# Kernel tuning notes

Hardware: AMD Instinct MI355X
Metric: run time of the kernel (lower is better)

Reference implementation:

```python
import jax, jax.numpy as jnp
import numpy as np

D_MODEL = 2048
H_TOTAL = 32
D_HEAD = D_MODEL // H_TOTAL  # 64
H_ACTIVE = 4
ROPE_BASE = 10000.0


def _apply_rope(t, cos, sin):
    # t: [B, H, T, DH]; cos/sin: [T, DH//2]; interleaved pair rotation
    t1 = t[..., 0::2]
    t2 = t[..., 1::2]
    r1 = t1 * cos - t2 * sin
    r2 = t1 * sin + t2 * cos
    return jnp.stack([r1, r2], axis=-1).reshape(t.shape)


def setup_inputs() -> dict:
    key = jax.random.key(0)
    ks = jax.random.split(key, 4)
    x = jax.random.normal(ks[0], (4, 1024, D_MODEL), dtype=jnp.float32)
    w_router = jax.random.normal(ks[1], (D_MODEL, H_TOTAL), dtype=jnp.float32) * 0.02
    w_qkv = jax.random.normal(ks[2], (D_MODEL, 3 * D_MODEL), dtype=jnp.float32) * 0.02
    w_out = jax.random.normal(ks[3], (D_MODEL, D_MODEL), dtype=jnp.float32) * 0.02
    return {"x": x, "w_router": w_router, "w_qkv": w_qkv, "w_out": w_out}


def reference(x, w_router, w_qkv, w_out):
    B, T, _ = x.shape
    # --- SwitchRouter: per-token probabilities over heads ---
    probs = jax.nn.softmax(x @ w_router, axis=-1)            # [B, T, H]
    # top-h_active heads per token (dense-math equivalent of sparse dispatch)
    _, top_idx = jax.lax.top_k(probs, H_ACTIVE)              # [B, T, HA]
    mask = jnp.sum(jax.nn.one_hot(top_idx, H_TOTAL, dtype=x.dtype), axis=-2)  # [B, T, H]
    gate = probs * mask                                      # router-scored gate

    # --- QKV projection ---
    qkv = x @ w_qkv                                          # [B, T, 3D]
    q, k, v = jnp.split(qkv, 3, axis=-1)
    def to_heads(t):
        return t.reshape(B, T, H_TOTAL, D_HEAD).transpose(0, 2, 1, 3)  # [B, H, T, DH]
    q, k, v = to_heads(q), to_heads(k), to_heads(v)

    # --- RoPE ---
    inv_freq = 1.0 / (ROPE_BASE ** (jnp.arange(0, D_HEAD, 2, dtype=jnp.float32) / D_HEAD))
    ang = jnp.arange(T, dtype=jnp.float32)[:, None] * inv_freq[None, :]  # [T, DH/2]
    cos, sin = jnp.cos(ang), jnp.sin(ang)
    q = _apply_rope(q, cos, sin)
    k = _apply_rope(k, cos, sin)

    # --- causal SDPA ---
    scores = jnp.einsum('bhqd,bhkd->bhqk', q, k) / np.float32(np.sqrt(D_HEAD))
    causal = jnp.tril(jnp.ones((T, T), dtype=bool))
    scores = jnp.where(causal, scores, jnp.finfo(scores.dtype).min)
    attn = jax.nn.softmax(scores, axis=-1)
    out = jnp.einsum('bhqk,bhkd->bhqd', attn, v)             # [B, H, T, DH]

    # --- gate: only active heads contribute (scatter-back equivalent) ---
    out = out * gate.transpose(0, 2, 1)[..., None]           # [B, H, T, DH]
    out = out.transpose(0, 2, 1, 3).reshape(B, T, D_MODEL)
    return out @ w_out
```

## Files before the change

### kernel.cpp

```cpp
#include <hip/hip_runtime.h>
#include <hip/hip_bf16.h>
#include <stdint.h>
#include <stddef.h>

typedef __attribute__((ext_vector_type(8))) short bf16x8;
typedef __attribute__((ext_vector_type(8))) unsigned short u16x8;
typedef __attribute__((ext_vector_type(4))) float f32x4;

#define TT 1024

__device__ __forceinline__ unsigned short f2bf(float f){
  unsigned u = __builtin_bit_cast(unsigned, f);
  unsigned r = 0x7fffu + ((u >> 16) & 1u);
  return (unsigned short)((u + r) >> 16);
}
__device__ __forceinline__ float bf2f(unsigned short s){
  unsigned u = ((unsigned)s) << 16;
  return __builtin_bit_cast(float, u);
}
__device__ __forceinline__ void gload16(const unsigned short* g, unsigned short* l){
  __builtin_amdgcn_global_load_lds(
      (const __attribute__((address_space(1))) void*)g,
      (__attribute__((address_space(3))) void*)l, 16, 0, 0);
}

__global__ void transpose_cast_kernel(const float* __restrict__ in, unsigned short* __restrict__ out,
                                      int R, int C){
  __shared__ float tile[32][33];
  int c0 = blockIdx.x * 32, r0 = blockIdx.y * 32;
  for (int i = threadIdx.y; i < 32; i += 8)
    tile[i][threadIdx.x] = in[(size_t)(r0 + i) * C + c0 + threadIdx.x];
  __syncthreads();
  for (int i = threadIdx.y; i < 32; i += 8)
    out[(size_t)(c0 + i) * R + r0 + threadIdx.x] = f2bf(tile[threadIdx.x][i]);
}

__global__ void rope_table_kernel(float* __restrict__ tab){
  int idx = blockIdx.x * 256 + threadIdx.x;
  int pos = idx >> 5, i = idx & 31;
  float freq = powf(10000.0f, -(float)i / 32.0f);
  float ang = (float)pos * freq;
  tab[idx * 2]     = cosf(ang);
  tab[idx * 2 + 1] = sinf(ang);
}

__global__ __launch_bounds__(256) void prep_kernel(const float* __restrict__ x,
                                                   const float* __restrict__ wr,
                                                   unsigned short* __restrict__ x_bf,
                                                   float* __restrict__ gate){
  __shared__ float xc[8 * 256];
  __shared__ float red[8 * 8 * 32];
  const int tid = threadIdx.x;
  const int tok0 = blockIdx.x * 8;
  const int p = tid >> 5, h = tid & 31;
  float acc[8] = {0.f,0.f,0.f,0.f,0.f,0.f,0.f,0.f};

  for (int kb = 0; kb < 8; kb++){
    __syncthreads();
    {
      int tok = tid >> 5, e = (tid & 31) * 8;
      const float* xp = x + (size_t)(tok0 + tok) * 2048 + kb * 256 + e;
      float4 v0 = *(const float4*)xp, v1 = *(const float4*)(xp + 4);
      float vals[8] = {v0.x, v0.y, v0.z, v0.w, v1.x, v1.y, v1.z, v1.w};
      u16x8 ob;
      #pragma unroll
      for (int jj = 0; jj < 8; jj++) ob[jj] = f2bf(vals[jj]);
      *(u16x8*)(x_bf + (size_t)(tok0 + tok) * 2048 + kb * 256 + e) = ob;
      #pragma unroll
      for (int jj = 0; jj < 8; jj++) xc[tok * 256 + e + jj] = vals[jj];
    }
    __syncthreads();
    const float* wp = wr + (size_t)(kb * 256 + p * 32) * 32 + h;
    #pragma unroll 4
    for (int j = 0; j < 32; j++){
      float wv = wp[j * 32];
      #pragma unroll
      for (int tok = 0; tok < 8; tok++)
        acc[tok] += xc[tok * 256 + p * 32 + j] * wv;
    }
  }
  #pragma unroll
  for (int tok = 0; tok < 8; tok++) red[(p * 8 + tok) * 32 + h] = acc[tok];
  __syncthreads();
  {
    int lane = tid & 63;
    int tok = (tid >> 6) * 2 + (lane >> 5);
    int hh = lane & 31;
    float logit = 0.f;
    #pragma unroll
    for (int pp = 0; pp < 8; pp++) logit += red[(pp * 8 + tok) * 32 + hh];
    float m = logit;
    #pragma unroll
    for (int s = 16; s >= 1; s >>= 1) m = fmaxf(m, __shfl_xor(m, s));
    float e = __expf(logit - m);
    float sum = e;
    #pragma unroll
    for (int s = 16; s >= 1; s >>= 1) sum += __shfl_xor(sum, s);
    float prob = e / sum;
    float v = logit; int sel = 0;
    #pragma unroll
    for (int rr2 = 0; rr2 < 4; rr2++){
      float bv = v; int bi = hh;
      #pragma unroll
      for (int s = 16; s >= 1; s >>= 1){
        float ov = __shfl_xor(bv, s); int oi = __shfl_xor(bi, s);
        if (ov > bv || (ov == bv && oi < bi)) { bv = ov; bi = oi; }
      }
      if (hh == bi) { sel = 1; v = -3.4e38f; }
    }
    gate[(size_t)(tok0 + tok) * 32 + hh] = sel ? prob : 0.f;
  }
}

__global__ void compact_kernel(const float* __restrict__ gate, int* __restrict__ idx,
                               int* __restrict__ counts){
  int bh = blockIdx.x;
  int b = bh >> 5, h = bh & 31;
  int lane = threadIdx.x;
  int base = 0;
  for (int c = 0; c < 16; c++){
    int t = c * 64 + lane;
    bool act = gate[(size_t)(b * TT + t) * 32 + h] != 0.f;
    unsigned long long mask = __ballot(act);
    int pos = base + __popcll(mask & ((1ull << lane) - 1ull));
    if (act) idx[bh * TT + pos] = t;
    base += __popcll(mask);
  }
  if (lane == 0) counts[bh] = base;
}

#define MFMA_B16(a, b, c) __builtin_amdgcn_mfma_f32_16x16x32_bf16((a), (b), (c), 0, 0, 0)

template<int EPI>
__global__ __launch_bounds__(512, 2) void gemm8(const unsigned short* __restrict__ A,
                                                const unsigned short* __restrict__ Bt,
                                                float* __restrict__ Cf,
                                                unsigned short* __restrict__ qk,
                                                unsigned short* __restrict__ vt,
                                                const float* __restrict__ tab,
                                                int N, int K, int nbn){
  extern __shared__ unsigned short smem[];
  unsigned short* SA = smem;
  unsigned short* SB = smem + 49152;

  const int nblk = gridDim.x;
  int raw = blockIdx.x;
  int tile = (raw & 7) * (nblk >> 3) + (raw >> 3);
  const int bm = tile / nbn, bn = tile % nbn;

  const int tid = threadIdx.x, lane = tid & 63, wid = tid >> 6;
  const int wrow = wid >> 1, wcol = wid & 1;
  const int li = lane & 15, lg = lane >> 4;
  const int swz = (li & 7) << 4;

  const int aoff0 = (((wrow * 64 + li) * 128) + ((lg * 16) ^ swz)) >> 1;
  const int aoff1 = (((wrow * 64 + li) * 128) + ((64 + lg * 16) ^ swz)) >> 1;
  const int boff0 = (((wcol * 64 + li) * 128) + ((lg * 16) ^ swz)) >> 1;
  const int boff1 = (((wcol * 64 + li) * 128) + ((64 + lg * 16) ^ swz)) >> 1;

  int L0 = tid * 16,            r0_ = L0 >> 7, c0_ = (L0 & 127) ^ ((r0_ & 7) << 4);
  int L1 = 8192 + tid * 16,     r1_ = L1 >> 7, c1_ = (L1 & 127) ^ ((r1_ & 7) << 4);
  int L2 = 16384 + tid * 16,    r2_ = L2 >> 7, c2_ = (L2 & 127) ^ ((r2_ & 7) << 4);
  int L3 = 24576 + tid * 16,    r3_ = L3 >> 7, c3_ = (L3 & 127) ^ ((r3_ & 7) << 4);
  const unsigned short* gA0p = A + (size_t)(bm * 256 + r0_) * K + (c0_ >> 1);
  const unsigned short* gA1p = A + (size_t)(bm * 256 + r1_) * K + (c1_ >> 1);
  const unsigned short* gA2p = A + (size_t)(bm * 256 + r2_) * K + (c2_ >> 1);
  const unsigned short* gA3p = A + (size_t)(bm * 256 + r3_) * K + (c3_ >> 1);
  const unsigned short* gB0p = Bt + (size_t)(bn * 128 + r0_) * K + (c0_ >> 1);
  const unsigned short* gB1p = Bt + (size_t)(bn * 128 + r1_) * K + (c1_ >> 1);
  const int aL0 = L0 >> 1, aL1 = L1 >> 1, aL2 = L2 >> 1, aL3 = L3 >> 1;

  auto stageA0 = [&](int tt){ unsigned short* b = SA + (tt % 3) * 16384;
    gload16(gA0p + (size_t)tt * 64, b + aL0);
    gload16(gA1p + (size_t)tt * 64, b + aL1); };
  auto stageA1 = [&](int tt){ unsigned short* b = SA + (tt % 3) * 16384;
    gload16(gA2p + (size_t)tt * 64, b + aL2);
    gload16(gA3p + (size_t)tt * 64, b + aL3); };
  auto stageB = [&](int tt){ unsigned short* b = SB + (tt % 3) * 8192;
    gload16(gB0p + (size_t)tt * 64, b + aL0);
    gload16(gB1p + (size_t)tt * 64, b + aL1); };

  f32x4 acc[4][4];
  #pragma unroll
  for (int i = 0; i < 4; i++)
    #pragma unroll
    for (int j = 0; j < 4; j++) acc[i][j] = f32x4{0.f, 0.f, 0.f, 0.f};

  const int NT = K >> 6;
  stageA0(0); stageA1(0); stageB(0);
  stageA0(1); stageA1(1); stageB(1);

  for (int t = 0; t < NT; ++t){
    if (t < NT - 1) asm volatile("s_waitcnt vmcnt(6)" ::: "memory");
    else            asm volatile("s_waitcnt vmcnt(0)" ::: "memory");
    __builtin_amdgcn_s_barrier();
    __builtin_amdgcn_sched_barrier(0);
    const unsigned short* as = SA + (t % 3) * 16384;
    const unsigned short* bs = SB + (t % 3) * 8192;
    const bool st = (t + 2 < NT);
    bf16x8 a0, a1, a2, a3, b0, b1, b2, b3;

    a0 = *(const bf16x8*)(as + aoff0);
    a1 = *(const bf16x8*)(as + aoff0 + 1024);
    b0 = *(const bf16x8*)(bs + boff0);
    b1 = *(const bf16x8*)(bs + boff0 + 1024);
    b2 = *(const bf16x8*)(bs + boff0 + 2048);
    b3 = *(const bf16x8*)(bs + boff0 + 3072);
    if (st) stageA0(t + 2);
    __builtin_amdgcn_s_barrier();
    asm volatile("s_waitcnt lgkmcnt(0)" ::: "memory");
    __builtin_amdgcn_sched_barrier(0);
    __builtin_amdgcn_s_setprio(1);
    acc[0][0] = MFMA_B16(a0, b0, acc[0][0]); acc[0][1] = MFMA_B16(a0, b1, acc[0][1]);
    acc[0][2] = MFMA_B16(a0, b2, acc[0][2]); acc[0][3] = MFMA_B16(a0, b3, acc[0][3]);
    acc[1][0] = MFMA_B16(a1, b0, acc[1][0]); acc[1][1] = MFMA_B16(a1, b1, acc[1][1]);
    acc[1][2] = MFMA_B16(a1, b2, acc[1][2]); acc[1][3] = MFMA_B16(a1, b3, acc[1][3]);
    __builtin_amdgcn_s_setprio(0);
    __builtin_amdgcn_s_barrier();

    a2 = *(const bf16x8*)(as + aoff0 + 2048);
    a3 = *(const bf16x8*)(as + aoff0 + 3072);
    if (st) stageA1(t + 2);
    __builtin_amdgcn_s_barrier();
    asm volatile("s_waitcnt lgkmcnt(0)" ::: "memory");
    __builtin_amdgcn_sched_barrier(0);
    __builtin_amdgcn_s_setprio(1);
    acc[2][0] = MFMA_B16(a2, b0, acc[2][0]); acc[2][1] = MFMA_B16(a2, b1, acc[2][1]);
    acc[2][2] = MFMA_B16(a2, b2, acc[2][2]); acc[2][3] = MFMA_B16(a2, b3, acc[2][3]);
    acc[3][0] = MFMA_B16(a3, b0, acc[3][0]); acc[3][1] = MFMA_B16(a3, b1, acc[3][1]);
    acc[3][2] = MFMA_B16(a3, b2, acc[3][2]); acc[3][3] = MFMA_B16(a3, b3, acc[3][3]);
    __builtin_amdgcn_s_setprio(0);
    __builtin_amdgcn_s_barrier();

    a0 = *(const bf16x8*)(as + aoff1);
    a1 = *(const bf16x8*)(as + aoff1 + 1024);
    b0 = *(const bf16x8*)(bs + boff1);
    b1 = *(const bf16x8*)(bs + boff1 + 1024);
    b2 = *(const bf16x8*)(bs + boff1 + 2048);
    b3 = *(const bf16x8*)(bs + boff1 + 3072);
    if (st) stageB(t + 2);
    __builtin_amdgcn_s_barrier();
    asm volatile("s_waitcnt lgkmcnt(0)" ::: "memory");
    __builtin_amdgcn_sched_barrier(0);
    __builtin_amdgcn_s_setprio(1);
    acc[0][0] = MFMA_B16(a0, b0, acc[0][0]); acc[0][1] = MFMA_B16(a0, b1, acc[0][1]);
    acc[0][2] = MFMA_B16(a0, b2, acc[0][2]); acc[0][3] = MFMA_B16(a0, b3, acc[0][3]);
    acc[1][0] = MFMA_B16(a1, b0, acc[1][0]); acc[1][1] = MFMA_B16(a1, b1, acc[1][1]);
    acc[1][2] = MFMA_B16(a1, b2, acc[1][2]); acc[1][3] = MFMA_B16(a1, b3, acc[1][3]);
    __builtin_amdgcn_s_setprio(0);
    __builtin_amdgcn_s_barrier();

    a2 = *(const bf16x8*)(as + aoff1 + 2048);
    a3 = *(const bf16x8*)(as + aoff1 + 3072);
    __builtin_amdgcn_s_barrier();
    asm volatile("s_waitcnt lgkmcnt(0)" ::: "memory");
    __builtin_amdgcn_sched_barrier(0);
    __builtin_amdgcn_s_setprio(1);
    acc[2][0] = MFMA_B16(a2, b0, acc[2][0]); acc[2][1] = MFMA_B16(a2, b1, acc[2][1]);
    acc[2][2] = MFMA_B16(a2, b2, acc[2][2]); acc[2][3] = MFMA_B16(a2, b3, acc[2][3]);
    acc[3][0] = MFMA_B16(a3, b0, acc[3][0]); acc[3][1] = MFMA_B16(a3, b1, acc[3][1]);
    acc[3][2] = MFMA_B16(a3, b2, acc[3][2]); acc[3][3] = MFMA_B16(a3, b3, acc[3][3]);
    __builtin_amdgcn_s_setprio(0);
  }

  if (EPI == 1){
    const int colbase = bn * 128 + wcol * 64;
    if (bn < 32){
      #pragma unroll
      for (int i = 0; i < 4; i++){
        #pragma unroll
        for (int j = 0; j < 4; j++){
          int col = colbase + j * 16 + li;
          int ii = (col & 63) >> 1;
          #pragma unroll
          for (int r = 0; r < 4; r++){
            int row = bm * 256 + wrow * 64 + i * 16 + lg * 4 + r;
            int pos = row & (TT - 1);
            const float* tp = tab + ((size_t)pos * 32 + ii) * 2;
            float c = tp[0], s = tp[1];
            float val = acc[i][j][r];
            float pv = __shfl_xor(val, 1);
            float res = (li & 1) ? (pv * s + val * c) : (val * c - pv * s);
            qk[(size_t)row * 4096 + col] = f2bf(res);
          }
        }
      }
    } else {
      #pragma unroll
      for (int i = 0; i < 4; i++){
        #pragma unroll
        for (int j = 0; j < 4; j++){
          int vcol = colbase + j * 16 + li - 4096;
          int hh = vcol >> 6, d = vcol & 63;
          int row0 = bm * 256 + wrow * 64 + i * 16 + lg * 4;
          int b = row0 >> 10, t0 = row0 & (TT - 1);
          ushort4 pk;
          pk.x = f2bf(acc[i][j][0]); pk.y = f2bf(acc[i][j][1]);
          pk.z = f2bf(acc[i][j][2]); pk.w = f2bf(acc[i][j][3]);
          *(ushort4*)(vt + ((size_t)((b * 32 + hh) * 64 + d)) * TT + t0) = pk;
        }
      }
    }
  } else {
    #pragma unroll
    for (int i = 0; i < 4; i++)
      #pragma unroll
      for (int j = 0; j < 4; j++)
        #pragma unroll
        for (int r = 0; r < 4; r++){
          size_t row = (size_t)(bm * 256 + wrow * 64 + i * 16 + lg * 4 + r);
          size_t col = (size_t)(bn * 128 + wcol * 64 + j * 16 + li);
          Cf[row * N + col] = acc[i][j][r];
        }
  }
}

__global__ __launch_bounds__(256) void attn_sparse_kernel(const unsigned short* __restrict__ qk,
                                                          const unsigned short* __restrict__ vt,
                                                          const float* __restrict__ gate,
                                                          const int* __restrict__ idx,
                                                          const int* __restrict__ counts,
                                                          unsigned short* __restrict__ attn_out){
  __shared__ unsigned short Ks[64 * 64];
  __shared__ unsigned short Vs[64 * 64];
  __shared__ unsigned short Ps[4][16 * 64];
  const int bh = blockIdx.x, qt = blockIdx.y;
  const int count = counts[bh];
  if (qt * 64 >= count) return;
  const int b = bh >> 5, h = bh & 31;
  const int tid = threadIdx.x, lane = tid & 63, w = tid >> 6;
  const int li = lane & 15, lg = lane >> 4;
  const int* myidx = idx + bh * TT + qt * 64;
  const int nvalid = min(64, count - qt * 64);
  const int qmax = myidx[nvalid - 1];

  int qi[4];
  #pragma unroll
  for (int r = 0; r < 4; r++){
    int s = w * 16 + lg * 4 + r;
    qi[r] = (s < nvalid) ? myidx[s] : -1;
  }
  int qrow = (w * 16 + li < nvalid) ? myidx[w * 16 + li] : 0;
  bf16x8 qf0, qf1;
  {
    const unsigned short* qp = qk + (size_t)(b * TT + qrow) * 4096 + h * 64;
    qf0 = *(const bf16x8*)(qp + lg * 8);
    qf1 = *(const bf16x8*)(qp + 32 + lg * 8);
  }
  f32x4 o[4];
  #pragma unroll
  for (int i = 0; i < 4; i++) o[i] = f32x4{0.f, 0.f, 0.f, 0.f};
  float m_run[4], l_run[4];
  #pragma unroll
  for (int r = 0; r < 4; r++){ m_run[r] = -1e30f; l_run[r] = 0.f; }

  const int nkt = (qmax >> 6) + 1;
  for (int kt = 0; kt < nkt; kt++){
    const int kb = kt * 64;
    #pragma unroll
    for (int s2 = 0; s2 < 2; s2++){
      int s = s2 * 256 + tid;
      int r = s >> 3, c = (s & 7) * 8;
      gload16(qk + (size_t)(b * TT + kb + r) * 4096 + 2048 + h * 64 + c, &Ks[s * 8]);
      gload16(vt + (size_t)(bh * 64 + r) * TT + kb + c, &Vs[s * 8]);
    }
    __syncthreads();

    f32x4 s4[4];
    #pragma unroll
    for (int ni = 0; ni < 4; ni++){
      bf16x8 k0 = *(const bf16x8*)(&Ks[(ni * 16 + li) * 64 + lg * 8]);
      bf16x8 k1 = *(const bf16x8*)(&Ks[(ni * 16 + li) * 64 + 32 + lg * 8]);
      f32x4 t = f32x4{0.f, 0.f, 0.f, 0.f};
      t = MFMA_B16(qf0, k0, t);
      t = MFMA_B16(qf1, k1, t);
      s4[ni] = t;
    }
    float mt[4];
    #pragma unroll
    for (int r = 0; r < 4; r++) mt[r] = -1e30f;
    #pragma unroll
    for (int ni = 0; ni < 4; ni++){
      int kidx = kb + ni * 16 + li;
      #pragma unroll
      for (int r = 0; r < 4; r++){
        float val = s4[ni][r] * 0.125f;
        val = (kidx <= qi[r]) ? val : -1e30f;
        s4[ni][r] = val;
        mt[r] = fmaxf(mt[r], val);
      }
    }
    #pragma unroll
    for (int r = 0; r < 4; r++){
      #pragma unroll
      for (int sh = 8; sh >= 1; sh >>= 1) mt[r] = fmaxf(mt[r], __shfl_xor(mt[r], sh));
      float mnew = fmaxf(m_run[r], mt[r]);
      float corr = __expf(m_run[r] - mnew);
      m_run[r] = mnew;
      l_run[r] *= corr;
      #pragma unroll
      for (int j = 0; j < 4; j++) o[j][r] *= corr;
    }
    float rs[4] = {0.f, 0.f, 0.f, 0.f};
    #pragma unroll
    for (int ni = 0; ni < 4; ni++)
      #pragma unroll
      for (int r = 0; r < 4; r++){
        float p = __expf(s4[ni][r] - m_run[r]);
        s4[ni][r] = p;
        rs[r] += p;
      }
    #pragma unroll
    for (int r = 0; r < 4; r++){
      #pragma unroll
      for (int sh = 8; sh >= 1; sh >>= 1) rs[r] += __shfl_xor(rs[r], sh);
      l_run[r] += rs[r];
    }
    #pragma unroll
    for (int ni = 0; ni < 4; ni++)
      #pragma unroll
      for (int r = 0; r < 4; r++)
        Ps[w][(lg * 4 + r) * 64 + ni * 16 + li] = f2bf(s4[ni][r]);
    #pragma unroll
    for (int ks = 0; ks < 2; ks++){
      bf16x8 pa = *(const bf16x8*)(&Ps[w][li * 64 + ks * 32 + lg * 8]);
      #pragma unroll
      for (int ni = 0; ni < 4; ni++){
        bf16x8 vb = *(const bf16x8*)(&Vs[(ni * 16 + li) * 64 + ks * 32 + lg * 8]);
        o[ni] = MFMA_B16(pa, vb, o[ni]);
      }
    }
    __syncthreads();
  }
  #pragma unroll
  for (int r = 0; r < 4; r++){
    if (qi[r] < 0) continue;
    float g = gate[(size_t)(b * TT + qi[r]) * 32 + h];
    float inv = g / l_run[r];
    #pragma unroll
    for (int ni = 0; ni < 4; ni++)
      attn_out[(size_t)(b * TT + qi[r]) * 2048 + h * 64 + ni * 16 + li] = f2bf(o[ni][r] * inv);
  }
}

extern "C" void kernel_launch(void* const* d_in, const int* in_sizes, int n_in,
                              void* d_out, int out_size, void* d_ws, size_t ws_size,
                              hipStream_t stream){
  const float* x        = (const float*)d_in[0];
  const float* w_router = (const float*)d_in[1];
  const float* w_qkv    = (const float*)d_in[2];
  const float* w_out    = (const float*)d_in[3];
  float* out = (float*)d_out;
  char* ws = (char*)d_ws;

  unsigned short* qk    = (unsigned short*)(ws);
  unsigned short* vt    = (unsigned short*)(ws + 33554432);
  unsigned short* x_bf  = (unsigned short*)(ws + 50331648);
  unsigned short* wqkvT = (unsigned short*)(ws + 67108864);
  unsigned short* woutT = (unsigned short*)(ws + 92274688);
  float* gate           = (float*)(ws + 100663296);
  float* tab            = (float*)(ws + 101187584);
  unsigned short* attn  = x_bf;
  int* idx              = (int*)(ws + 67108864);
  int* counts           = (int*)(ws + 67633152);

  constexpr int GEMM_LDS = 147456;
  (void)hipFuncSetAttribute(reinterpret_cast<const void*>(&gemm8<1>),
                            hipFuncAttributeMaxDynamicSharedMemorySize, GEMM_LDS);
  (void)hipFuncSetAttribute(reinterpret_cast<const void*>(&gemm8<0>),
                            hipFuncAttributeMaxDynamicSharedMemorySize, GEMM_LDS);

  hipLaunchKernelGGL(transpose_cast_kernel, dim3(192, 64), dim3(32, 8), 0, stream, w_qkv, wqkvT, 2048, 6144);
  hipLaunchKernelGGL(transpose_cast_kernel, dim3(64, 64), dim3(32, 8), 0, stream, w_out, woutT, 2048, 2048);
  hipLaunchKernelGGL(rope_table_kernel, dim3(128), dim3(256), 0, stream, tab);
  hipLaunchKernelGGL(prep_kernel, dim3(512), dim3(256), 0, stream, x, w_router, x_bf, gate);
  hipLaunchKernelGGL((gemm8<1>), dim3(768), dim3(512), GEMM_LDS, stream,
                     x_bf, wqkvT, (float*)nullptr, qk, vt, tab, 6144, 2048, 48);
  hipLaunchKernelGGL(compact_kernel, dim3(128), dim3(64), 0, stream, gate, idx, counts);
  (void)hipMemsetAsync(attn, 0, (size_t)4096 * 2048 * 2, stream);
  hipLaunchKernelGGL(attn_sparse_kernel, dim3(128, 16), dim3(256), 0, stream, qk, vt, gate, idx, counts, attn);
  hipLaunchKernelGGL((gemm8<0>), dim3(256), dim3(512), GEMM_LDS, stream,
                     attn, woutT, out, (unsigned short*)nullptr, (unsigned short*)nullptr,
                     (const float*)nullptr, 2048, 2048, 16);
}
```

Measured before the change: 262.8 us.

## Rewrite GEMM with 32x32x16 MFMA, 4 waves per block, column-major tile order

Replaces the 8-wave 16x16x32 MFMA GEMM with a 4-wave kernel that uses 32x32x16 bf16 MFMAs. Each wave now covers a 128x64 sub-tile, and the K loop runs as four k-steps per 64-wide slab, with global-to-LDS staging spread across those steps. Tile ordering changes so blocks walk M fastest within an N column, and the epilogues are reworked for the 32x32 accumulator layout. The aim is fewer LDS reads per FLOP and better B-tile reuse in L2. In exchange it lowers waves per CU and removes the fine-grained barrier and priority scheduling, which may expose load latency.

```diff
diff --git a/kernel.cpp b/kernel.cpp
--- a/kernel.cpp
+++ b/kernel.cpp
@@ -6,6 +6,7 @@
 typedef __attribute__((ext_vector_type(8))) short bf16x8;
 typedef __attribute__((ext_vector_type(8))) unsigned short u16x8;
 typedef __attribute__((ext_vector_type(4))) float f32x4;
+typedef __attribute__((ext_vector_type(16))) float f32x16;
 
 #define TT 1024
 
@@ -129,159 +130,128 @@
   if (lane == 0) counts[bh] = base;
 }
 
-#define MFMA_B16(a, b, c) __builtin_amdgcn_mfma_f32_16x16x32_bf16((a), (b), (c), 0, 0, 0)
+#define MFMA32(a, b, c) __builtin_amdgcn_mfma_f32_32x32x16_bf16((a), (b), (c), 0, 0, 0)
 
 template<int EPI>
-__global__ __launch_bounds__(512, 2) void gemm8(const unsigned short* __restrict__ A,
-                                                const unsigned short* __restrict__ Bt,
-                                                float* __restrict__ Cf,
-                                                unsigned short* __restrict__ qk,
-                                                unsigned short* __restrict__ vt,
-                                                const float* __restrict__ tab,
-                                                int N, int K, int nbn){
+__global__ __launch_bounds__(256, 1) void gemm32(const unsigned short* __restrict__ A,
+                                                 const unsigned short* __restrict__ Bt,
+                                                 float* __restrict__ Cf,
+                                                 unsigned short* __restrict__ qk,
+                                                 unsigned short* __restrict__ vt,
+                                                 const float* __restrict__ tab,
+                                                 int N, int K, int nbm){
   extern __shared__ unsigned short smem[];
-  unsigned short* SA = smem;
-  unsigned short* SB = smem + 49152;
 
   const int nblk = gridDim.x;
-  int raw = blockIdx.x;
-  int tile = (raw & 7) * (nblk >> 3) + (raw >> 3);
-  const int bm = tile / nbn, bn = tile % nbn;
+  const int raw = blockIdx.x;
+  const int tile = (raw & 7) * (nblk >> 3) + (raw >> 3);
+  const int bn = tile / nbm, bm = tile % nbm;
 
   const int tid = threadIdx.x, lane = tid & 63, wid = tid >> 6;
   const int wrow = wid >> 1, wcol = wid & 1;
-  const int li = lane & 15, lg = lane >> 4;
-  const int swz = (li & 7) << 4;
-
-  const int aoff0 = (((wrow * 64 + li) * 128) + ((lg * 16) ^ swz)) >> 1;
-  const int aoff1 = (((wrow * 64 + li) * 128) + ((64 + lg * 16) ^ swz)) >> 1;
-  const int boff0 = (((wcol * 64 + li) * 128) + ((lg * 16) ^ swz)) >> 1;
-  const int boff1 = (((wcol * 64 + li) * 128) + ((64 + lg * 16) ^ swz)) >> 1;
-
-  int L0 = tid * 16,            r0_ = L0 >> 7, c0_ = (L0 & 127) ^ ((r0_ & 7) << 4);
-  int L1 = 8192 + tid * 16,     r1_ = L1 >> 7, c1_ = (L1 & 127) ^ ((r1_ & 7) << 4);
-  int L2 = 16384 + tid * 16,    r2_ = L2 >> 7, c2_ = (L2 & 127) ^ ((r2_ & 7) << 4);
-  int L3 = 24576 + tid * 16,    r3_ = L3 >> 7, c3_ = (L3 & 127) ^ ((r3_ & 7) << 4);
-  const unsigned short* gA0p = A + (size_t)(bm * 256 + r0_) * K + (c0_ >> 1);
-  const unsigned short* gA1p = A + (size_t)(bm * 256 + r1_) * K + (c1_ >> 1);
-  const unsigned short* gA2p = A + (size_t)(bm * 256 + r2_) * K + (c2_ >> 1);
-  const unsigned short* gA3p = A + (size_t)(bm * 256 + r3_) * K + (c3_ >> 1);
-  const unsigned short* gB0p = Bt + (size_t)(bn * 128 + r0_) * K + (c0_ >> 1);
-  const unsigned short* gB1p = Bt + (size_t)(bn * 128 + r1_) * K + (c1_ >> 1);
-  const int aL0 = L0 >> 1, aL1 = L1 >> 1, aL2 = L2 >> 1, aL3 = L3 >> 1;
-
-  auto stageA0 = [&](int tt){ unsigned short* b = SA + (tt % 3) * 16384;
-    gload16(gA0p + (size_t)tt * 64, b + aL0);
-    gload16(gA1p + (size_t)tt * 64, b + aL1); };
-  auto stageA1 = [&](int tt){ unsigned short* b = SA + (tt % 3) * 16384;
-    gload16(gA2p + (size_t)tt * 64, b + aL2);
-    gload16(gA3p + (size_t)tt * 64, b + aL3); };
-  auto stageB = [&](int tt){ unsigned short* b = SB + (tt % 3) * 8192;
-    gload16(gB0p + (size_t)tt * 64, b + aL0);
-    gload16(gB1p + (size_t)tt * 64, b + aL1); };
-
-  f32x4 acc[4][4];
+  const int l31 = lane & 31, hi = lane >> 5;
+  const int X = (l31 & 7) << 4;
+
+  const unsigned short* gA[8];
+  const unsigned short* gB[4];
+  #pragma unroll
+  for (int p = 0; p < 8; p++){
+    int L = tid * 16 + p * 4096;
+    int r = L >> 7, c = (L & 127) ^ ((r & 7) << 4);
+    gA[p] = A + (size_t)(bm * 256 + r) * K + (c >> 1);
+  }
+  #pragma unroll
+  for (int p = 0; p < 4; p++){
+    int L = tid * 16 + p * 4096;
+    int r = L >> 7, c = (L & 127) ^ ((r & 7) << 4);
+    gB[p] = Bt + (size_t)(bn * 128 + r) * K + (c >> 1);
+  }
+
+  auto stageA0 = [&](int tt){
+    unsigned short* b = smem + (tt % 3) * 24576;
+    size_t ko = (size_t)tt * 64;
+    gload16(gA[0] + ko, b + tid * 8);
+    gload16(gA[1] + ko, b + tid * 8 + 2048);
+    gload16(gA[2] + ko, b + tid * 8 + 4096);
+    gload16(gA[3] + ko, b + tid * 8 + 6144);
+  };
+  auto stageA1 = [&](int tt){
+    unsigned short* b = smem + (tt % 3) * 24576;
+    size_t ko = (size_t)tt * 64;
+    gload16(gA[4] + ko, b + tid * 8 + 8192);
+    gload16(gA[5] + ko, b + tid * 8 + 10240);
+    gload16(gA[6] + ko, b + tid * 8 + 12288);
+    gload16(gA[7] + ko, b + tid * 8 + 14336);
+  };
+  auto stageB = [&](int tt){
+    unsigned short* b = smem + (tt % 3) * 24576 + 16384;
+    size_t ko = (size_t)tt * 64;
+    gload16(gB[0] + ko, b + tid * 8);
+    gload16(gB[1] + ko, b + tid * 8 + 2048);
+    gload16(gB[2] + ko, b + tid * 8 + 4096);
+    gload16(gB[3] + ko, b + tid * 8 + 6144);
+  };
+
+  f32x16 acc[4][2];
   #pragma unroll
   for (int i = 0; i < 4; i++)
     #pragma unroll
-    for (int j = 0; j < 4; j++) acc[i][j] = f32x4{0.f, 0.f, 0.f, 0.f};
+    for (int j = 0; j < 2; j++) acc[i][j] = f32x16{0,0,0,0,0,0,0,0,0,0,0,0,0,0,0,0};
 
   const int NT = K >> 6;
   stageA0(0); stageA1(0); stageB(0);
   stageA0(1); stageA1(1); stageB(1);
 
+  const int arow = (wrow * 128 + l31) * 64;
+  const int brow = 16384 + (wcol * 64 + l31) * 64;
+
   for (int t = 0; t < NT; ++t){
-    if (t < NT - 1) asm volatile("s_waitcnt vmcnt(6)" ::: "memory");
+    if (t < NT - 1) asm volatile("s_waitcnt vmcnt(12)" ::: "memory");
     else            asm volatile("s_waitcnt vmcnt(0)" ::: "memory");
     __builtin_amdgcn_s_barrier();
     __builtin_amdgcn_sched_barrier(0);
-    const unsigned short* as = SA + (t % 3) * 16384;
-    const unsigned short* bs = SB + (t % 3) * 8192;
+    const unsigned short* bs = smem + (t % 3) * 24576;
     const bool st = (t + 2 < NT);
-    bf16x8 a0, a1, a2, a3, b0, b1, b2, b3;
-
-    a0 = *(const bf16x8*)(as + aoff0);
-    a1 = *(const bf16x8*)(as + aoff0 + 1024);
-    b0 = *(const bf16x8*)(bs + boff0);
-    b1 = *(const bf16x8*)(bs + boff0 + 1024);
-    b2 = *(const bf16x8*)(bs + boff0 + 2048);
-    b3 = *(const bf16x8*)(bs + boff0 + 3072);
-    if (st) stageA0(t + 2);
-    __builtin_amdgcn_s_barrier();
-    asm volatile("s_waitcnt lgkmcnt(0)" ::: "memory");
-    __builtin_amdgcn_sched_barrier(0);
-    __builtin_amdgcn_s_setprio(1);
-    acc[0][0] = MFMA_B16(a0, b0, acc[0][0]); acc[0][1] = MFMA_B16(a0, b1, acc[0][1]);
-    acc[0][2] = MFMA_B16(a0, b2, acc[0][2]); acc[0][3] = MFMA_B16(a0, b3, acc[0][3]);
-    acc[1][0] = MFMA_B16(a1, b0, acc[1][0]); acc[1][1] = MFMA_B16(a1, b1, acc[1][1]);
-    acc[1][2] = MFMA_B16(a1, b2, acc[1][2]); acc[1][3] = MFMA_B16(a1, b3, acc[1][3]);
-    __builtin_amdgcn_s_setprio(0);
-    __builtin_amdgcn_s_barrier();
-
-    a2 = *(const bf16x8*)(as + aoff0 + 2048);
-    a3 = *(const bf16x8*)(as + aoff0 + 3072);
-    if (st) stageA1(t + 2);
-    __builtin_amdgcn_s_barrier();
-    asm volatile("s_waitcnt lgkmcnt(0)" ::: "memory");
-    __builtin_amdgcn_sched_barrier(0);
-    __builtin_amdgcn_s_setprio(1);
-    acc[2][0] = MFMA_B16(a2, b0, acc[2][0]); acc[2][1] = MFMA_B16(a2, b1, acc[2][1]);
-    acc[2][2] = MFMA_B16(a2, b2, acc[2][2]); acc[2][3] = MFMA_B16(a2, b3, acc[2][3]);
-    acc[3][0] = MFMA_B16(a3, b0, acc[3][0]); acc[3][1] = MFMA_B16(a3, b1, acc[3][1]);
-    acc[3][2] = MFMA_B16(a3, b2, acc[3][2]); acc[3][3] = MFMA_B16(a3, b3, acc[3][3]);
-    __builtin_amdgcn_s_setprio(0);
-    __builtin_amdgcn_s_barrier();
-
-    a0 = *(const bf16x8*)(as + aoff1);
-    a1 = *(const bf16x8*)(as + aoff1 + 1024);
-    b0 = *(const bf16x8*)(bs + boff1);
-    b1 = *(const bf16x8*)(bs + boff1 + 1024);
-    b2 = *(const bf16x8*)(bs + boff1 + 2048);
-    b3 = *(const bf16x8*)(bs + boff1 + 3072);
-    if (st) stageB(t + 2);
-    __builtin_amdgcn_s_barrier();
-    asm volatile("s_waitcnt lgkmcnt(0)" ::: "memory");
-    __builtin_amdgcn_sched_barrier(0);
-    __builtin_amdgcn_s_setprio(1);
-    acc[0][0] = MFMA_B16(a0, b0, acc[0][0]); acc[0][1] = MFMA_B16(a0, b1, acc[0][1]);
-    acc[0][2] = MFMA_B16(a0, b2, acc[0][2]); acc[0][3] = MFMA_B16(a0, b3, acc[0][3]);
-    acc[1][0] = MFMA_B16(a1, b0, acc[1][0]); acc[1][1] = MFMA_B16(a1, b1, acc[1][1]);
-    acc[1][2] = MFMA_B16(a1, b2, acc[1][2]); acc[1][3] = MFMA_B16(a1, b3, acc[1][3]);
-    __builtin_amdgcn_s_setprio(0);
-    __builtin_amdgcn_s_barrier();
-
-    a2 = *(const bf16x8*)(as + aoff1 + 2048);
-    a3 = *(const bf16x8*)(as + aoff1 + 3072);
-    __builtin_amdgcn_s_barrier();
-    asm volatile("s_waitcnt lgkmcnt(0)" ::: "memory");
-    __builtin_amdgcn_sched_barrier(0);
-    __builtin_amdgcn_s_setprio(1);
-    acc[2][0] = MFMA_B16(a2, b0, acc[2][0]); acc[2][1] = MFMA_B16(a2, b1, acc[2][1]);
-    acc[2][2] = MFMA_B16(a2, b2, acc[2][2]); acc[2][3] = MFMA_B16(a2, b3, acc[2][3]);
-    acc[3][0] = MFMA_B16(a3, b0, acc[3][0]); acc[3][1] = MFMA_B16(a3, b1, acc[3][1]);
-    acc[3][2] = MFMA_B16(a3, b2, acc[3][2]); acc[3][3] = MFMA_B16(a3, b3, acc[3][3]);
-    __builtin_amdgcn_s_setprio(0);
+    #pragma unroll
+    for (int ks = 0; ks < 4; ks++){
+      const int kp = ((ks * 32 + hi * 16) ^ X) >> 1;
+      bf16x8 a0 = *(const bf16x8*)(bs + arow +        kp);
+      bf16x8 a1 = *(const bf16x8*)(bs + arow + 2048 + kp);
+      bf16x8 a2 = *(const bf16x8*)(bs + arow + 4096 + kp);
+      bf16x8 a3 = *(const bf16x8*)(bs + arow + 6144 + kp);
+      bf16x8 b0 = *(const bf16x8*)(bs + brow +        kp);
+      bf16x8 b1 = *(const bf16x8*)(bs + brow + 2048 + kp);
+      if (st && ks == 0) stageA0(t + 2);
+      if (st && ks == 1) stageA1(t + 2);
+      if (st && ks == 2) stageB(t + 2);
+      acc[0][0] = MFMA32(a0, b0, acc[0][0]); acc[0][1] = MFMA32(a0, b1, acc[0][1]);
+      acc[1][0] = MFMA32(a1, b0, acc[1][0]); acc[1][1] = MFMA32(a1, b1, acc[1][1]);
+      acc[2][0] = MFMA32(a2, b0, acc[2][0]); acc[2][1] = MFMA32(a2, b1, acc[2][1]);
+      acc[3][0] = MFMA32(a3, b0, acc[3][0]); acc[3][1] = MFMA32(a3, b1, acc[3][1]);
+    }
   }
 
   if (EPI == 1){
-    const int colbase = bn * 128 + wcol * 64;
     if (bn < 32){
       #pragma unroll
       for (int i = 0; i < 4; i++){
         #pragma unroll
-        for (int j = 0; j < 4; j++){
-          int col = colbase + j * 16 + li;
+        for (int j = 0; j < 2; j++){
+          int col = bn * 128 + wcol * 64 + j * 32 + l31;
           int ii = (col & 63) >> 1;
           #pragma unroll
-          for (int r = 0; r < 4; r++){
-            int row = bm * 256 + wrow * 64 + i * 16 + lg * 4 + r;
-            int pos = row & (TT - 1);
-            const float* tp = tab + ((size_t)pos * 32 + ii) * 2;
-            float c = tp[0], s = tp[1];
-            float val = acc[i][j][r];
-            float pv = __shfl_xor(val, 1);
-            float res = (li & 1) ? (pv * s + val * c) : (val * c - pv * s);
-            qk[(size_t)row * 4096 + col] = f2bf(res);
+          for (int g = 0; g < 4; g++){
+            #pragma unroll
+            for (int rr = 0; rr < 4; rr++){
+              int row = bm * 256 + wrow * 128 + i * 32 + g * 8 + hi * 4 + rr;
+              int pos = row & (TT - 1);
+              const float* tp = tab + ((size_t)pos * 32 + ii) * 2;
+              float c = tp[0], s = tp[1];
+              float val = acc[i][j][g * 4 + rr];
+              float pv = __shfl_xor(val, 1);
+              float res = (lane & 1) ? (pv * s + val * c) : (val * c - pv * s);
+              qk[(size_t)row * 4096 + col] = f2bf(res);
+            }
           }
         }
       }
@@ -289,32 +259,41 @@
       #pragma unroll
       for (int i = 0; i < 4; i++){
         #pragma unroll
-        for (int j = 0; j < 4; j++){
-          int vcol = colbase + j * 16 + li - 4096;
+        for (int j = 0; j < 2; j++){
+          int vcol = bn * 128 + wcol * 64 + j * 32 + l31 - 4096;
           int hh = vcol >> 6, d = vcol & 63;
-          int row0 = bm * 256 + wrow * 64 + i * 16 + lg * 4;
+          int row0 = bm * 256 + wrow * 128 + i * 32 + hi * 4;
           int b = row0 >> 10, t0 = row0 & (TT - 1);
-          ushort4 pk;
-          pk.x = f2bf(acc[i][j][0]); pk.y = f2bf(acc[i][j][1]);
-          pk.z = f2bf(acc[i][j][2]); pk.w = f2bf(acc[i][j][3]);
-          *(ushort4*)(vt + ((size_t)((b * 32 + hh) * 64 + d)) * TT + t0) = pk;
+          #pragma unroll
+          for (int g = 0; g < 4; g++){
+            ushort4 pk;
+            pk.x = f2bf(acc[i][j][g * 4 + 0]); pk.y = f2bf(acc[i][j][g * 4 + 1]);
+            pk.z = f2bf(acc[i][j][g * 4 + 2]); pk.w = f2bf(acc[i][j][g * 4 + 3]);
+            *(ushort4*)(vt + ((size_t)((b * 32 + hh) * 64 + d)) * TT + t0 + g * 8) = pk;
+          }
         }
       }
     }
   } else {
     #pragma unroll
-    for (int i = 0; i < 4; i++)
-      #pragma unroll
-      for (int j = 0; j < 4; j++)
+    for (int i = 0; i < 4; i++){
+      #pragma unroll
+      for (int j = 0; j < 2; j++){
+        int col = bn * 128 + wcol * 64 + j * 32 + l31;
         #pragma unroll
-        for (int r = 0; r < 4; r++){
-          size_t row = (size_t)(bm * 256 + wrow * 64 + i * 16 + lg * 4 + r);
-          size_t col = (size_t)(bn * 128 + wcol * 64 + j * 16 + li);
-          Cf[row * N + col] = acc[i][j][r];
+        for (int g = 0; g < 4; g++){
+          #pragma unroll
+          for (int rr = 0; rr < 4; rr++){
+            size_t row = (size_t)(bm * 256 + wrow * 128 + i * 32 + g * 8 + hi * 4 + rr);
+            Cf[row * N + col] = acc[i][j][g * 4 + rr];
+          }
         }
-  }
-}
-
+      }
+    }
+  }
+}
+
+#define MFMA_B16(a, b, c) __builtin_amdgcn_mfma_f32_16x16x32_bf16((a), (b), (c), 0, 0, 0)
 __global__ __launch_bounds__(256) void attn_sparse_kernel(const unsigned short* __restrict__ qk,
                                                           const unsigned short* __restrict__ vt,
                                                           const float* __restrict__ gate,
@@ -465,21 +444,21 @@
   int* counts           = (int*)(ws + 67633152);
 
   constexpr int GEMM_LDS = 147456;
-  (void)hipFuncSetAttribute(reinterpret_cast<const void*>(&gemm8<1>),
+  (void)hipFuncSetAttribute(reinterpret_cast<const void*>(&gemm32<1>),
                             hipFuncAttributeMaxDynamicSharedMemorySize, GEMM_LDS);
-  (void)hipFuncSetAttribute(reinterpret_cast<const void*>(&gemm8<0>),
+  (void)hipFuncSetAttribute(reinterpret_cast<const void*>(&gemm32<0>),
                             hipFuncAttributeMaxDynamicSharedMemorySize, GEMM_LDS);
 
   hipLaunchKernelGGL(transpose_cast_kernel, dim3(192, 64), dim3(32, 8), 0, stream, w_qkv, wqkvT, 2048, 6144);
   hipLaunchKernelGGL(transpose_cast_kernel, dim3(64, 64), dim3(32, 8), 0, stream, w_out, woutT, 2048, 2048);
   hipLaunchKernelGGL(rope_table_kernel, dim3(128), dim3(256), 0, stream, tab);
   hipLaunchKernelGGL(prep_kernel, dim3(512), dim3(256), 0, stream, x, w_router, x_bf, gate);
-  hipLaunchKernelGGL((gemm8<1>), dim3(768), dim3(512), GEMM_LDS, stream,
-                     x_bf, wqkvT, (float*)nullptr, qk, vt, tab, 6144, 2048, 48);
+  hipLaunchKernelGGL((gemm32<1>), dim3(768), dim3(256), GEMM_LDS, stream,
+                     x_bf, wqkvT, (float*)nullptr, qk, vt, tab, 6144, 2048, 16);
   hipLaunchKernelGGL(compact_kernel, dim3(128), dim3(64), 0, stream, gate, idx, counts);
   (void)hipMemsetAsync(attn, 0, (size_t)4096 * 2048 * 2, stream);
   hipLaunchKernelGGL(attn_sparse_kernel, dim3(128, 16), dim3(256), 0, stream, qk, vt, gate, idx, counts, attn);
-  hipLaunchKernelGGL((gemm8<0>), dim3(256), dim3(512), GEMM_LDS, stream,
+  hipLaunchKernelGGL((gemm32<0>), dim3(256), dim3(256), GEMM_LDS, stream,
                      attn, woutT, out, (unsigned short*)nullptr, (unsigned short*)nullptr,
                      (const float*)nullptr, 2048, 2048, 16);
 }
```

Result: slower. 270.1 us (+2.8%).
